# Kernel tuning notes

Hardware: AMD Instinct MI355X
Metric: run time of the kernel (lower is better)

## Reference

```python
import jax, jax.numpy as jnp
import numpy as np

N_SENT = 100000   # source ('sent') nodes
N_TYPE = 10000    # destination ('type') nodes
E = 640000        # edges of etype 'has'
D = 128           # out_dim
LEAKY_SLOPE = 0.01  # F.leaky_relu default


def setup_inputs() -> dict:
    key = jax.random.key(0)
    k0, k1, k2, k3, k4 = jax.random.split(key, 5)
    h_sent = jax.random.normal(k0, (N_SENT, D), jnp.float32)
    h_type = jax.random.normal(k1, (N_TYPE, D), jnp.float32)
    # attn_fc: Linear(2*D, 1, bias=False) -> weight [1, 2*D]
    attn_w = jax.random.normal(k2, (1, 2 * D), jnp.float32) * (1.0 / np.sqrt(2 * D))
    src_idx = jax.random.randint(k3, (E,), 0, N_SENT, dtype=jnp.int32)
    dst_idx = jax.random.randint(k4, (E,), 0, N_TYPE, dtype=jnp.int32)
    return {"h_sent": h_sent, "h_type": h_type, "attn_w": attn_w,
            "src_idx": src_idx, "dst_idx": dst_idx}


def reference(h_sent, h_type, attn_w, src_idx, dst_idx):
    w = attn_w[0]  # [2D]
    # attn_fc(cat(src_h, dst_h)) == src_h @ w[:D] + dst_h @ w[D:]  (no bias)
    s_src = h_sent @ w[:D]   # [N_SENT]
    s_dst = h_type @ w[D:]   # [N_TYPE]
    e = jax.nn.leaky_relu(s_src[src_idx] + s_dst[dst_idx], LEAKY_SLOPE)  # [E]
    # segment (per-destination) softmax over incoming edges
    m = jax.ops.segment_max(e, dst_idx, num_segments=N_TYPE)             # [N_TYPE]
    m = jnp.where(jnp.isfinite(m), m, 0.0)                               # empty segments -> 0
    ex = jnp.exp(e - m[dst_idx])                                         # [E]
    denom = jax.ops.segment_sum(ex, dst_idx, num_segments=N_TYPE)        # [N_TYPE]
    alpha = ex / denom[dst_idx]                                          # [E]
    # weighted scatter-sum of source features into destination nodes
    msg = alpha[:, None] * h_sent[src_idx]                               # [E, D]
    h_new = jax.ops.segment_sum(msg, dst_idx, num_segments=N_TYPE)       # [N_TYPE, D]
    # DGL only updates nodes that received messages; isolated nodes keep h
    deg = jax.ops.segment_sum(jnp.ones_like(e), dst_idx, num_segments=N_TYPE)
    return jnp.where(deg[:, None] > 0, h_new, h_type)
```

## Files before the change

### kernel.cpp

```cpp
#include <hip/hip_runtime.h>
#include <stdint.h>
#include <stddef.h>

#define N_SENT 100000
#define N_TYPE 10000
#define NEDGE  640000
#define NROWS  (N_SENT + N_TYPE)
#define MAXDEG 256
#define HB     64
#define HCHUNK (NEDGE / HB)

__device__ __forceinline__ float bf2f(uint32_t lo16) {
    return __builtin_bit_cast(float, lo16 << 16);
}
__device__ __forceinline__ uint32_t f2bf(float f) {
    uint32_t u = __builtin_bit_cast(uint32_t, f);
    return (u + 0x7fffu + ((u >> 16) & 1u)) >> 16;
}

__device__ __forceinline__ bool detect_bf16(const uint32_t* __restrict__ h) {
    uint32_t u = h[threadIdx.x & 63];
    uint32_t e_lo = (u >> 7) & 0xffu;
    int ok = (e_lo >= 100u && e_lo <= 140u) ? 1 : 0;
    unsigned long long m = __ballot(ok);
    return __popcll(m) >= 48;
}

#define SCORE_BLOCKS ((NROWS + 63) / 64)

__global__ __launch_bounds__(256) void scores_k(const void* __restrict__ h_sent,
                                                const void* __restrict__ h_type,
                                                const void* __restrict__ attn_w,
                                                float* __restrict__ s_src,
                                                float* __restrict__ s_dst) {
    int lane = threadIdx.x & 63;
    int r0   = (blockIdx.x * 4 + (int)(threadIdx.x >> 6)) * 16;
    bool isbf = detect_bf16((const uint32_t*)h_sent);
    float v[16];
    if (isbf) {
        uint32_t wv_s = ((const uint32_t*)attn_w)[lane];
        uint32_t wv_t = ((const uint32_t*)attn_w)[64 + lane];
        float ws0 = bf2f(wv_s & 0xffffu), ws1 = bf2f(wv_s >> 16);
        float wt0 = bf2f(wv_t & 0xffffu), wt1 = bf2f(wv_t >> 16);
#pragma unroll
        for (int i = 0; i < 16; i++) {
            int g = r0 + i;
            if (g >= NROWS) { v[i] = 0.0f; continue; }
            bool isSrc = g < N_SENT;
            const uint32_t* hp = isSrc
                ? (const uint32_t*)h_sent + (size_t)g * 64
                : (const uint32_t*)h_type + (size_t)(g - N_SENT) * 64;
            uint32_t hv = hp[lane];
            v[i] = isSrc ? (bf2f(hv & 0xffffu) * ws0 + bf2f(hv >> 16) * ws1)
                         : (bf2f(hv & 0xffffu) * wt0 + bf2f(hv >> 16) * wt1);
        }
    } else {
        float2 wv_s = ((const float2*)attn_w)[lane];
        float2 wv_t = ((const float2*)attn_w)[64 + lane];
#pragma unroll
        for (int i = 0; i < 16; i++) {
            int g = r0 + i;
            if (g >= NROWS) { v[i] = 0.0f; continue; }
            bool isSrc = g < N_SENT;
            const float2* hp = isSrc
                ? (const float2*)h_sent + (size_t)g * 64
                : (const float2*)h_type + (size_t)(g - N_SENT) * 64;
            float2 hv = hp[lane];
            v[i] = isSrc ? (hv.x * wv_s.x + hv.y * wv_s.y)
                         : (hv.x * wv_t.x + hv.y * wv_t.y);
        }
    }
    int b0 = lane & 1, b1 = (lane >> 1) & 1, b2 = (lane >> 2) & 1, b3 = (lane >> 3) & 1;
    float w_[8];
#pragma unroll
    for (int i = 0; i < 8; i++) {
        float keep = b0 ? v[2 * i + 1] : v[2 * i];
        float send = b0 ? v[2 * i]     : v[2 * i + 1];
        w_[i] = keep + __shfl_xor(send, 1, 64);
    }
    float x_[4];
#pragma unroll
    for (int i = 0; i < 4; i++) {
        float keep = b1 ? w_[2 * i + 1] : w_[2 * i];
        float send = b1 ? w_[2 * i]     : w_[2 * i + 1];
        x_[i] = keep + __shfl_xor(send, 2, 64);
    }
    float y_[2];
#pragma unroll
    for (int i = 0; i < 2; i++) {
        float keep = b2 ? x_[2 * i + 1] : x_[2 * i];
        float send = b2 ? x_[2 * i]     : x_[2 * i + 1];
        y_[i] = keep + __shfl_xor(send, 4, 64);
    }
    float z;
    {
        float keep = b3 ? y_[1] : y_[0];
        float send = b3 ? y_[0] : y_[1];
        z = keep + __shfl_xor(send, 8, 64);
    }
    z += __shfl_xor(z, 16, 64);
    z += __shfl_xor(z, 32, 64);
    if (lane < 16) {
        int g = r0 + lane;
        if (g < NROWS) {
            if (g < N_SENT) s_src[g] = z;
            else            s_dst[g - N_SENT] = z;
        }
    }
}

__global__ __launch_bounds__(256) void count_k(const int* __restrict__ dst,
                                               uint32_t* __restrict__ count2) {
    __shared__ uint32_t hist[N_TYPE];
    int cb = blockIdx.x;
    int t  = threadIdx.x;
    for (int i = t; i < N_TYPE; i += 256) hist[i] = 0u;
    __syncthreads();
    int e0 = cb * HCHUNK;
    for (int i = t; i < HCHUNK; i += 256)
        atomicAdd(&hist[dst[e0 + i]], 1u);
    __syncthreads();
    uint32_t* row = count2 + (size_t)cb * N_TYPE;
    for (int i = t; i < N_TYPE; i += 256) row[i] = hist[i];
}

__global__ __launch_bounds__(256) void sumscan_k(uint32_t* __restrict__ count2,
                                                 uint32_t* __restrict__ total) {
    int b = blockIdx.x * 256 + threadIdx.x;
    if (b >= N_TYPE) return;
    uint32_t run = 0;
#pragma unroll 4
    for (int c = 0; c < HB; c++) {
        uint32_t* p = count2 + (size_t)c * N_TYPE + b;
        uint32_t v = *p;
        *p = run;
        run += v;
    }
    total[b] = run;
}

__global__ __launch_bounds__(1024) void scan_k(const uint32_t* __restrict__ total,
                                               uint32_t* __restrict__ offsets) {
    const int CH = 10;
    int t = threadIdx.x, lane = t & 63, wv = t >> 6;
    int base = t * CH;
    uint32_t local[CH];
    uint32_t tsum = 0;
#pragma unroll
    for (int i = 0; i < CH; i++) {
        int idx = base + i;
        uint32_t c = (idx < N_TYPE) ? total[idx] : 0u;
        local[i] = c;
        tsum += c;
    }
    uint32_t orig = tsum;
#pragma unroll
    for (int off = 1; off < 64; off <<= 1) {
        uint32_t v = __shfl_up(tsum, off, 64);
        if (lane >= off) tsum += v;
    }
    __shared__ uint32_t wsum[16];
    if (lane == 63) wsum[wv] = tsum;
    __syncthreads();
    if (wv == 0 && lane < 16) {
        uint32_t u = wsum[lane], o = u;
#pragma unroll
        for (int off = 1; off < 16; off <<= 1) {
            uint32_t v = __shfl_up(u, off, 64);
            if (lane >= off) u += v;
        }
        wsum[lane] = u - o;
    }
    __syncthreads();
    uint32_t run = wsum[wv] + tsum - orig;
#pragma unroll
    for (int i = 0; i < CH; i++) {
        int idx = base + i;
        if (idx < N_TYPE) {
            offsets[idx] = run;
            run += local[i];
        } else if (idx == N_TYPE) {
            offsets[idx] = run;
        }
    }
}

__global__ __launch_bounds__(256) void fill_k(const int* __restrict__ src,
                                              const int* __restrict__ dst,
                                              const uint32_t* __restrict__ offsets,
                                              const uint32_t* __restrict__ base2,
                                              uint32_t* __restrict__ edge_src) {
    __shared__ uint32_t cur[N_TYPE];
    int cb = blockIdx.x;
    int t  = threadIdx.x;
    const uint32_t* brow = base2 + (size_t)cb * N_TYPE;
    for (int i = t; i < N_TYPE; i += 256) cur[i] = offsets[i] + brow[i];
    __syncthreads();
    int e0 = cb * HCHUNK;
    for (int i = t; i < HCHUNK; i += 256) {
        int e = e0 + i;
        uint32_t pos = atomicAdd(&cur[dst[e]], 1u);
        edge_src[pos] = (uint32_t)src[e];
    }
}

__global__ __launch_bounds__(256) void agg_k(const void* __restrict__ h_sent,
                                             const void* __restrict__ h_type,
                                             const float* __restrict__ s_src,
                                             const float* __restrict__ s_dst,
                                             const uint32_t* __restrict__ offsets,
                                             const uint32_t* __restrict__ edge_src,
                                             void* __restrict__ out) {
    __shared__ float    sc[4][MAXDEG];
    __shared__ uint32_t ss[4][MAXDEG];
    int j     = (blockIdx.x * 256 + threadIdx.x) >> 6;
    int wslot = threadIdx.x >> 6;
    int lane  = threadIdx.x & 63;
    bool valid = j < N_TYPE;
    bool isbf  = detect_bf16((const uint32_t*)h_sent);
    uint32_t beg = 0, deg = 0;
    float sdj = 0.0f;
    if (valid) {
        beg = offsets[j];
        deg = offsets[j + 1] - beg;
        sdj = s_dst[j];
    }
    float*    mysc = sc[wslot];
    uint32_t* myss = ss[wslot];
    bool fits = (deg <= MAXDEG);
    float m = -INFINITY;
    for (uint32_t k = lane; k < deg; k += 64) {
        uint32_t s = edge_src[beg + k];
        float v = s_src[s] + sdj;
        v = v > 0.0f ? v : 0.01f * v;
        if (fits) { mysc[k] = v; myss[k] = s; }
        m = fmaxf(m, v);
    }
#pragma unroll
    for (int off = 32; off; off >>= 1) m = fmaxf(m, __shfl_xor(m, off, 64));
    __syncthreads();
    if (!valid) return;
    if (deg == 0) {
        if (isbf) ((uint32_t*)out)[(size_t)j * 64 + lane] =
                      ((const uint32_t*)h_type)[(size_t)j * 64 + lane];
        else      ((float2*)out)[(size_t)j * 64 + lane] =
                      ((const float2*)h_type)[(size_t)j * 64 + lane];
        return;
    }
    float denom = 0.0f, a0 = 0.0f, a1 = 0.0f;
    if (isbf) {
        const uint32_t* hp = (const uint32_t*)h_sent;
        uint32_t k = 0;
        if (fits) {
            for (; k + 8 <= deg; k += 8) {
                uint32_t sv[8]; float vv[8]; uint32_t gv[8];
#pragma unroll
                for (int i = 0; i < 8; i++) { sv[i] = myss[k + i]; vv[i] = mysc[k + i]; }
#pragma unroll
                for (int i = 0; i < 8; i++) gv[i] = hp[(size_t)sv[i] * 64 + lane];
#pragma unroll
                for (int i = 0; i < 8; i++) {
                    float w = __expf(vv[i] - m);
                    denom += w;
                    a0 += w * bf2f(gv[i] & 0xffffu);
                    a1 += w * bf2f(gv[i] >> 16);
                }
            }
            for (; k < deg; ++k) {
                float w = __expf(mysc[k] - m);
                uint32_t g = hp[(size_t)myss[k] * 64 + lane];
                denom += w;
                a0 += w * bf2f(g & 0xffffu);
                a1 += w * bf2f(g >> 16);
            }
        } else {
            for (k = 0; k < deg; ++k) {
                uint32_t s = edge_src[beg + k];
                float v = s_src[s] + sdj; v = v > 0.0f ? v : 0.01f * v;
                float w = __expf(v - m);
                uint32_t g = hp[(size_t)s * 64 + lane];
                denom += w;
                a0 += w * bf2f(g & 0xffffu);
                a1 += w * bf2f(g >> 16);
            }
        }
        float inv = 1.0f / denom;
        ((uint32_t*)out)[(size_t)j * 64 + lane] = f2bf(a0 * inv) | (f2bf(a1 * inv) << 16);
    } else {
        const float2* hp = (const float2*)h_sent;
        uint32_t k = 0;
        if (fits) {
            for (; k + 8 <= deg; k += 8) {
                uint32_t sv[8]; float vv[8]; float2 gv[8];
#pragma unroll
                for (int i = 0; i < 8; i++) { sv[i] = myss[k + i]; vv[i] = mysc[k + i]; }
#pragma unroll
                for (int i = 0; i < 8; i++) gv[i] = hp[(size_t)sv[i] * 64 + lane];
#pragma unroll
                for (int i = 0; i < 8; i++) {
                    float w = __expf(vv[i] - m);
                    denom += w;
                    a0 += w * gv[i].x;
                    a1 += w * gv[i].y;
                }
            }
            for (; k < deg; ++k) {
                float w = __expf(mysc[k] - m);
                float2 g = hp[(size_t)myss[k] * 64 + lane];
                denom += w;
                a0 += w * g.x;
                a1 += w * g.y;
            }
        } else {
            for (k = 0; k < deg; ++k) {
                uint32_t s = edge_src[beg + k];
                float v = s_src[s] + sdj; v = v > 0.0f ? v : 0.01f * v;
                float w = __expf(v - m);
                float2 g = hp[(size_t)s * 64 + lane];
                denom += w;
                a0 += w * g.x;
                a1 += w * g.y;
            }
        }
        float inv = 1.0f / denom;
        ((float2*)out)[(size_t)j * 64 + lane] = make_float2(a0 * inv, a1 * inv);
    }
}

static inline size_t align_up(size_t x) { return (x + 255) & ~(size_t)255; }

extern "C" void kernel_launch(void* const* d_in, const int* in_sizes, int n_in,
                              void* d_out, int out_size, void* d_ws, size_t ws_size,
                              hipStream_t stream) {
    const void* h_sent = d_in[0];
    const void* h_type = d_in[1];
    const void* attn_w = d_in[2];
    const int* src_idx = (const int*)d_in[3];
    const int* dst_idx = (const int*)d_in[4];

    char* w = (char*)d_ws;
    float*    s_src     = (float*)w;    w += align_up((size_t)N_SENT * 4);
    float*    s_dst     = (float*)w;    w += align_up((size_t)N_TYPE * 4);
    uint32_t* count2    = (uint32_t*)w; w += align_up((size_t)HB * N_TYPE * 4);
    uint32_t* total     = (uint32_t*)w; w += align_up((size_t)N_TYPE * 4);
    uint32_t* offsets   = (uint32_t*)w; w += align_up((size_t)(N_TYPE + 1) * 4);
    uint32_t* edge_src  = (uint32_t*)w; w += align_up((size_t)NEDGE * 4);

    scores_k<<<SCORE_BLOCKS, 256, 0, stream>>>(h_sent, h_type, attn_w, s_src, s_dst);
    count_k<<<HB, 256, 0, stream>>>(dst_idx, count2);
    sumscan_k<<<(N_TYPE + 255) / 256, 256, 0, stream>>>(count2, total);
    scan_k<<<1, 1024, 0, stream>>>(total, offsets);
    fill_k<<<HB, 256, 0, stream>>>(src_idx, dst_idx, offsets, count2, edge_src);
    agg_k<<<(N_TYPE + 3) / 4, 256, 0, stream>>>(h_sent, h_type, s_src, s_dst,
                                                offsets, edge_src, d_out);
}
```

Baseline: 202.0 us.

## Fuse degree counting into score kernel and use global-atomic CSR fill

```diff
diff --git a/kernel.cpp b/kernel.cpp
--- a/kernel.cpp
+++ b/kernel.cpp
@@ -7,8 +7,6 @@
 #define NEDGE  640000
 #define NROWS  (N_SENT + N_TYPE)
 #define MAXDEG 256
-#define HB     64
-#define HCHUNK (NEDGE / HB)
 
 __device__ __forceinline__ float bf2f(uint32_t lo16) {
     return __builtin_bit_cast(float, lo16 << 16);
@@ -31,8 +29,10 @@
 __global__ __launch_bounds__(256) void scores_k(const void* __restrict__ h_sent,
                                                 const void* __restrict__ h_type,
                                                 const void* __restrict__ attn_w,
+                                                const int* __restrict__ dst,
                                                 float* __restrict__ s_src,
-                                                float* __restrict__ s_dst) {
+                                                float* __restrict__ s_dst,
+                                                uint32_t* __restrict__ total) {
     int lane = threadIdx.x & 63;
     int r0   = (blockIdx.x * 4 + (int)(threadIdx.x >> 6)) * 16;
     bool isbf = detect_bf16((const uint32_t*)h_sent);
@@ -81,7 +81,8 @@
     float x_[4];
 #pragma unroll
     for (int i = 0; i < 4; i++) {
-        float keep = b1 ? w_[2 * i + 1] : w_[2 * i];
+        float keep = b1 ? x_[0] * 0.0f + (b1 ? w_[2 * i + 1] : w_[2 * i]) : w_[2 * i];
+        keep = b1 ? w_[2 * i + 1] : w_[2 * i];
         float send = b1 ? w_[2 * i]     : w_[2 * i + 1];
         x_[i] = keep + __shfl_xor(send, 2, 64);
     }
@@ -107,40 +108,13 @@
             else            s_dst[g - N_SENT] = z;
         }
     }
-}
-
-__global__ __launch_bounds__(256) void count_k(const int* __restrict__ dst,
-                                               uint32_t* __restrict__ count2) {
-    __shared__ uint32_t hist[N_TYPE];
-    int cb = blockIdx.x;
-    int t  = threadIdx.x;
-    for (int i = t; i < N_TYPE; i += 256) hist[i] = 0u;
-    __syncthreads();
-    int e0 = cb * HCHUNK;
-    for (int i = t; i < HCHUNK; i += 256)
-        atomicAdd(&hist[dst[e0 + i]], 1u);
-    __syncthreads();
-    uint32_t* row = count2 + (size_t)cb * N_TYPE;
-    for (int i = t; i < N_TYPE; i += 256) row[i] = hist[i];
-}
-
-__global__ __launch_bounds__(256) void sumscan_k(uint32_t* __restrict__ count2,
-                                                 uint32_t* __restrict__ total) {
-    int b = blockIdx.x * 256 + threadIdx.x;
-    if (b >= N_TYPE) return;
-    uint32_t run = 0;
-#pragma unroll 4
-    for (int c = 0; c < HB; c++) {
-        uint32_t* p = count2 + (size_t)c * N_TYPE + b;
-        uint32_t v = *p;
-        *p = run;
-        run += v;
-    }
-    total[b] = run;
+    for (int e = blockIdx.x * 256 + (int)threadIdx.x; e < NEDGE; e += SCORE_BLOCKS * 256)
+        atomicAdd(total + dst[e], 1u);
 }
 
 __global__ __launch_bounds__(1024) void scan_k(const uint32_t* __restrict__ total,
-                                               uint32_t* __restrict__ offsets) {
+                                               uint32_t* __restrict__ offsets,
+                                               uint32_t* __restrict__ cursor) {
     const int CH = 10;
     int t = threadIdx.x, lane = t & 63, wv = t >> 6;
     int base = t * CH;
@@ -178,6 +152,7 @@
         int idx = base + i;
         if (idx < N_TYPE) {
             offsets[idx] = run;
+            cursor[idx]  = run;
             run += local[i];
         } else if (idx == N_TYPE) {
             offsets[idx] = run;
@@ -187,19 +162,11 @@
 
 __global__ __launch_bounds__(256) void fill_k(const int* __restrict__ src,
                                               const int* __restrict__ dst,
-                                              const uint32_t* __restrict__ offsets,
-                                              const uint32_t* __restrict__ base2,
+                                              uint32_t* __restrict__ cursor,
                                               uint32_t* __restrict__ edge_src) {
-    __shared__ uint32_t cur[N_TYPE];
-    int cb = blockIdx.x;
-    int t  = threadIdx.x;
-    const uint32_t* brow = base2 + (size_t)cb * N_TYPE;
-    for (int i = t; i < N_TYPE; i += 256) cur[i] = offsets[i] + brow[i];
-    __syncthreads();
-    int e0 = cb * HCHUNK;
-    for (int i = t; i < HCHUNK; i += 256) {
-        int e = e0 + i;
-        uint32_t pos = atomicAdd(&cur[dst[e]], 1u);
+    int e = blockIdx.x * 256 + (int)threadIdx.x;
+    if (e < NEDGE) {
+        uint32_t pos = atomicAdd(&cursor[dst[e]], 1u);
         edge_src[pos] = (uint32_t)src[e];
     }
 }
@@ -341,16 +308,16 @@
     char* w = (char*)d_ws;
     float*    s_src     = (float*)w;    w += align_up((size_t)N_SENT * 4);
     float*    s_dst     = (float*)w;    w += align_up((size_t)N_TYPE * 4);
-    uint32_t* count2    = (uint32_t*)w; w += align_up((size_t)HB * N_TYPE * 4);
     uint32_t* total     = (uint32_t*)w; w += align_up((size_t)N_TYPE * 4);
     uint32_t* offsets   = (uint32_t*)w; w += align_up((size_t)(N_TYPE + 1) * 4);
+    uint32_t* cursor    = (uint32_t*)w; w += align_up((size_t)N_TYPE * 4);
     uint32_t* edge_src  = (uint32_t*)w; w += align_up((size_t)NEDGE * 4);
 
-    scores_k<<<SCORE_BLOCKS, 256, 0, stream>>>(h_sent, h_type, attn_w, s_src, s_dst);
-    count_k<<<HB, 256, 0, stream>>>(dst_idx, count2);
-    sumscan_k<<<(N_TYPE + 255) / 256, 256, 0, stream>>>(count2, total);
-    scan_k<<<1, 1024, 0, stream>>>(total, offsets);
-    fill_k<<<HB, 256, 0, stream>>>(src_idx, dst_idx, offsets, count2, edge_src);
+    hipMemsetAsync(total, 0, (size_t)N_TYPE * 4, stream);
+    scores_k<<<SCORE_BLOCKS, 256, 0, stream>>>(h_sent, h_type, attn_w, dst_idx,
+                                               s_src, s_dst, total);
+    scan_k<<<1, 1024, 0, stream>>>(total, offsets, cursor);
+    fill_k<<<NEDGE / 256, 256, 0, stream>>>(src_idx, dst_idx, cursor, edge_src);
     agg_k<<<(N_TYPE + 3) / 4, 256, 0, stream>>>(h_sent, h_type, s_src, s_dst,
                                                 offsets, edge_src, d_out);
 }
```

Measured after the change: 231.9 us. +14.8%, slower.
